# Optimization experiments

Hardware: AMD Instinct MI355X
Metric: run time of the kernel (lower is better)

The kernel has to match this reference:

```python
import jax, jax.numpy as jnp
import numpy as np

_MASK = -1.0e9
_EPS = 1e-8
B, N, E, D, L, NREL, TAU = 4, 2048, 32768, 128, 3, 1000, 0.1


def setup_inputs() -> dict:
    key = jax.random.key(0)
    ks = jax.random.split(key, 24)
    s = 0.05
    inp = {
        'edge_index': jax.random.randint(ks[0], (B, 2, E), 0, N, dtype=jnp.int32),
        'rels': jax.random.randint(ks[1], (B, E), 0, NREL, dtype=jnp.int32),
        'scores': jax.random.uniform(ks[2], (B, E), dtype=jnp.float32),
        'edge_conf_mask': jax.random.randint(ks[3], (B, E), 0, 2) > 0,
        'edge_mask': jax.random.randint(ks[4], (B, E), 0, 2) > 0,
        'mask': jnp.ones((B, N), dtype=bool),
        'r_query_embed': jax.random.normal(ks[5], (B, D), dtype=jnp.float32),
        'conf_embeds': jax.random.normal(ks[6], (B, E, D), dtype=jnp.float32),
        'rel_table': jax.random.normal(ks[7], (NREL, D), dtype=jnp.float32) * s,
        'beta_W': jax.random.normal(ks[8], (D, 1), dtype=jnp.float32) * s,
        'beta_b': jnp.zeros((1,), dtype=jnp.float32),
        'msg_W': jax.random.normal(ks[9], (L, 5 * D, D), dtype=jnp.float32) * s,
        'msg_b': jnp.zeros((L, D), dtype=jnp.float32),
        'upd_W': jax.random.normal(ks[10], (L, D, D), dtype=jnp.float32) * s,
        'upd_b': jnp.zeros((L, D), dtype=jnp.float32),
        'ln_g': jnp.ones((D,), dtype=jnp.float32),
        'ln_b': jnp.zeros((D,), dtype=jnp.float32),
        'att_W': jax.random.normal(ks[11], (L, 3 * D, 1), dtype=jnp.float32) * s,
        'att_b': jnp.zeros((L, 1), dtype=jnp.float32),
        'den_W1': jax.random.normal(ks[12], (3 * D, D), dtype=jnp.float32) * s,
        'den_b1': jnp.zeros((D,), dtype=jnp.float32),
        'den_W2': jax.random.normal(ks[13], (D, 1), dtype=jnp.float32) * s,
        'den_b2': jnp.zeros((1,), dtype=jnp.float32),
    }
    return inp


def _layer_norm(x, g, b, eps=1e-5):
    mu = jnp.mean(x, axis=-1, keepdims=True)
    var = jnp.var(x, axis=-1, keepdims=True)
    return (x - mu) * jax.lax.rsqrt(var + eps) * g + b


def reference(edge_index, rels, scores, edge_conf_mask, edge_mask, mask,
              r_query_embed, conf_embeds, rel_table, beta_W, beta_b,
              msg_W, msg_b, upd_W, upd_b, ln_g, ln_b, att_W, att_b,
              den_W1, den_b1, den_W2, den_b2):
    Bb, Nn = mask.shape
    Ee = edge_index.shape[2]
    d = rel_table.shape[1]
    bidx = jnp.arange(Bb)[:, None]                      # [B,1] batch index for scatter/gather
    src = edge_index[:, 0, :]                           # [B,E]
    tgt = edge_index[:, 1, :]                           # [B,E]

    h_init = jnp.zeros((Bb, Nn, d), dtype=rel_table.dtype).at[:, 0, :].set(1.0)
    h = h_init
    h_r = rel_table[rels]                               # [B,E,D]
    rq = jnp.broadcast_to(r_query_embed[:, None, :], (Bb, Ee, d))
    em = edge_mask.astype(h.dtype)[..., None]           # [B,E,1]

    # edge denoiser gate
    gate_in = jnp.concatenate([h_r, rq, conf_embeds], axis=-1)
    den = jax.nn.sigmoid(jax.nn.relu(gate_in @ den_W1 + den_b1) @ den_W2 + den_b2) * em

    beta = jax.nn.sigmoid((h_r + rq) @ beta_W + beta_b)             # [B,E,1]
    gate_known = jax.nn.sigmoid((scores[..., None] - beta) / TAU)
    gate = jnp.where(edge_conf_mask[..., None], gate_known, 0.5)

    outs = []
    for k in range(msg_W.shape[0]):
        h_src = h[bidx, src]                            # [B,E,D] gather
        h_init_src = h_init[bidx, src]
        msg_in = jnp.concatenate([h_src * h_r, h_src, h_init_src, h_r, conf_embeds], axis=-1)
        raw_msg = jax.nn.relu(msg_in @ msg_W[k] + msg_b[k])         # [B,E,D]

        att_in = jnp.concatenate([raw_msg, h_r, rq], axis=-1)
        att = jax.nn.leaky_relu((att_in @ att_W[k] + att_b[k])[..., 0], 0.01)
        att = jnp.where(edge_mask, att, _MASK)

        # scatter-softmax over edges sharing a target node
        mx = jnp.full((Bb, Nn), _MASK, dtype=att.dtype).at[bidx, tgt].max(att)
        ex = jnp.exp(att - mx[bidx, tgt])
        sm = jnp.zeros((Bb, Nn), dtype=att.dtype).at[bidx, tgt].add(ex)
        alpha = ex / (sm[bidx, tgt] + _EPS)             # [B,E]

        wmsg = gate * alpha[..., None] * raw_msg * em * den
        aggr = jnp.zeros_like(h).at[bidx, tgt].add(wmsg)
        h = _layer_norm(h + aggr @ upd_W[k] + upd_b[k], ln_g, ln_b)
        outs.append(h[:, 0, :])
    return jnp.stack(outs, axis=1)                      # [B,L,D]
```

## Files before the change

### kernel.cpp

```cpp
#include <hip/hip_runtime.h>
#include <stdint.h>
#include <math.h>

#define BB 4
#define NNODE 2048
#define NE 32768
#define DDIM 128
#define NL 3
#define NRELS 1000
#define MASKV -1000000000.0f

typedef unsigned short ushort_t;
typedef __attribute__((ext_vector_type(8))) short bfrag;
typedef __attribute__((ext_vector_type(4))) float f4;

__device__ __forceinline__ float sigf(float x){ return 1.0f/(1.0f+expf(-x)); }

__device__ __forceinline__ float bf2f(ushort_t u){
  union { unsigned int i; float f; } v; v.i = ((unsigned int)u) << 16; return v.f;
}
__device__ __forceinline__ ushort_t f2bf(float x){
  union { float f; unsigned int u; } v; v.f = x;
  unsigned int r = (v.u + 0x7FFFu + ((v.u >> 16) & 1u)) >> 16;
  return (ushort_t)r;
}
__device__ __forceinline__ float bflo(unsigned u){
  union{unsigned i;float f;}v; v.i=u<<16; return v.f;
}
__device__ __forceinline__ float bfhi(unsigned u){
  union{unsigned i;float f;}v; v.i=u&0xFFFF0000u; return v.f;
}
__device__ __forceinline__ unsigned pmul_bf(unsigned a, unsigned b){
  return (unsigned)f2bf(bflo(a)*bflo(b)) | ((unsigned)f2bf(bfhi(a)*bfhi(b))<<16);
}
__device__ __forceinline__ unsigned packbf(float a, float b){
  return (unsigned)f2bf(a) | ((unsigned)f2bf(b)<<16);
}

__global__ void prep_kernel(const void* cm_raw, const void* em_raw,
    uint8_t* __restrict__ cm, uint8_t* __restrict__ em, int* __restrict__ deg,
    const float* __restrict__ relt, ushort_t* __restrict__ relt_bf,
    const float* __restrict__ rq,
    const float* __restrict__ attW, const float* __restrict__ betaW,
    const float* __restrict__ msgW, const float* __restrict__ denW1,
    const float* __restrict__ denb1,
    int* __restrict__ src_c, int* __restrict__ rel_c, int* __restrict__ ge_c,
    float* __restrict__ h, ushort_t* __restrict__ h_bf,
    ushort_t* __restrict__ img_msg, ushort_t* __restrict__ img_den,
    ushort_t* __restrict__ img_tab,
    float* __restrict__ att_rel, float* __restrict__ att_rq,
    float* __restrict__ beta_rel, float* __restrict__ beta_rq,
    float* __restrict__ denrq, float* __restrict__ initvec,
    float* __restrict__ src0vec)
{
  __shared__ int flag_s;
  if (threadIdx.x < 64){
    unsigned v = ((const unsigned*)cm_raw)[threadIdx.x];
    bool i32ok = (v <= 1u);
    bool f32ok = (v == 0u) || (v == 0x3F800000u);
    unsigned long long bi = __ballot(i32ok);
    unsigned long long bf_ = __ballot(f32ok);
    if (threadIdx.x == 0) flag_s = (bi==~0ULL) ? 0 : ((bf_==~0ULL) ? 1 : 2);
  }
  __syncthreads();
  const int f = flag_s;
  const int gid = blockIdx.x*256 + threadIdx.x;

  if (gid < BB*NE){
    uint8_t c, e;
    if (f == 0){ c = ((const int*)cm_raw)[gid]!=0;   e = ((const int*)em_raw)[gid]!=0; }
    else if (f == 1){ c = ((const float*)cm_raw)[gid]!=0.0f; e = ((const float*)em_raw)[gid]!=0.0f; }
    else { c = ((const uint8_t*)cm_raw)[gid]!=0; e = ((const uint8_t*)em_raw)[gid]!=0; }
    cm[gid]=c; em[gid]=e;
    src_c[gid]=0; rel_c[gid]=0; ge_c[gid]=0;
  }
  if (gid < BB*NNODE) deg[gid]=0;
  if (gid < NRELS*DDIM/4){
    float4 v = *(const float4*)&relt[gid*4];
    ushort4 o; o.x=f2bf(v.x); o.y=f2bf(v.y); o.z=f2bf(v.z); o.w=f2bf(v.w);
    *(ushort4*)&relt_bf[gid*4] = o;
  }
  {
    int base = gid*4;
    int nd = base & (NNODE*DDIM - 1);
    bool one = (nd < DDIM);
    float4 hv = one ? (float4){1.f,1.f,1.f,1.f} : (float4){0.f,0.f,0.f,0.f};
    ushort4 hb = one ? (ushort4){0x3F80,0x3F80,0x3F80,0x3F80} : (ushort4){0,0,0,0};
    *(float4*)&h[base] = hv;
    *(ushort4*)&h_bf[base] = hb;
  }
  if (gid < 22*8192){
    int img_id = gid >> 13;
    int ei = gid & 8191;
    int j = ei >> 6;
    int kk = (((ei & 63) << 1) ^ ((j & 7) << 4)) >> 1;
    float v; ushort_t* dst;
    if (img_id < 12){
      int k = img_id >> 2, c = img_id & 3;
      int rowbase = (c < 2) ? c*64 : 512 + (c-2)*64;
      v = msgW[(size_t)k*81920 + (rowbase+kk)*128 + j];
      dst = img_msg + (size_t)img_id*8192;
    } else if (img_id < 14){
      int c = img_id - 12;
      v = denW1[(size_t)(256 + c*64 + kk)*128 + j];
      dst = img_den + (size_t)c*8192;
    } else if (img_id < 20){
      int idx = img_id - 14, k = idx >> 1, c = idx & 1;
      v = msgW[(size_t)k*81920 + (384 + c*64 + kk)*128 + j];
      dst = img_tab + (size_t)idx*8192;
    } else {
      int c = img_id - 20;
      v = denW1[(size_t)(c*64 + kk)*128 + j];
      dst = img_tab + (size_t)(6+c)*8192;
    }
    dst[ei] = f2bf(v);
  }
  {
    int wid = gid >> 6;
    int lane = threadIdx.x & 63;
    if (wid < 4016){
      const float* vec; const float* w; float* dst; int di;
      if (wid < 3*NRELS){
        int k = wid/1000, rl = wid%1000;
        vec = relt + rl*DDIM; w = attW + k*384 + 128; dst = att_rel; di = wid;
      } else if (wid < 3*NRELS + 3*BB){
        int idx = wid - 3*NRELS; int k = idx/BB, b = idx%BB;
        vec = rq + b*DDIM; w = attW + k*384 + 256; dst = att_rq; di = idx;
      } else if (wid < 3*NRELS + 3*BB + NRELS){
        int rl = wid - (3*NRELS + 3*BB);
        vec = relt + rl*DDIM; w = betaW; dst = beta_rel; di = rl;
      } else {
        int b = wid - (3*NRELS + 3*BB + NRELS);
        vec = rq + b*DDIM; w = betaW; dst = beta_rq; di = b;
      }
      float s = vec[lane]*w[lane] + vec[lane+64]*w[lane+64];
      #pragma unroll
      for (int off=32; off; off>>=1) s += __shfl_xor(s, off, 64);
      if (lane == 0) dst[di] = s;
    } else if (wid < 4024){
      int widx = wid - 4016;
      const float* A = nullptr; const float* W; int K = 128;
      float* outp; const float* bias = nullptr;
      if (widx < 4){ A = rq + widx*128; W = denW1 + 16384; outp = denrq + widx*128; bias = denb1; }
      else if (widx < 7){ int k=widx-4; W = msgW + (size_t)k*81920 + 32768; outp = initvec + k*128; }
      else { W = msgW + 16384; K = 256; outp = src0vec; }
      float a0=0.f, a1=0.f;
      for (int kk=0; kk<K; kk+=8){
        float av[8], w0[8], w1[8];
        #pragma unroll
        for (int u=0;u<8;++u){
          av[u] = A ? A[kk+u] : 1.0f;
          w0[u] = W[(size_t)(kk+u)*128 + lane];
          w1[u] = W[(size_t)(kk+u)*128 + lane + 64];
        }
        #pragma unroll
        for (int u=0;u<8;++u){ a0 = fmaf(av[u], w0[u], a0); a1 = fmaf(av[u], w1[u], a1); }
      }
      if (bias){ a0 += bias[lane]; a1 += bias[lane+64]; }
      outp[lane] = a0; outp[lane+64] = a1;
    }
  }
}

__global__ void csr_hist_kernel(const int* __restrict__ edge_index,
                                const uint8_t* __restrict__ em, int* __restrict__ deg){
  int gid = blockIdx.x*256 + threadIdx.x;
  if (!em[gid]) return;
  int b = gid >> 15, e = gid & (NE-1);
  int tgt = edge_index[(b<<16) + NE + e];
  atomicAdd(&deg[(b<<11) + tgt], 1);
}
__global__ void csr_scan_kernel(const int* __restrict__ deg,
                                int* __restrict__ base, int* __restrict__ cursor){
  __shared__ int part[256];
  int t = threadIdx.x;
  int loc[32]; int s = 0;
  #pragma unroll
  for (int i=0;i<32;++i){ loc[i] = deg[t*32+i]; s += loc[i]; }
  part[t] = s; __syncthreads();
  for (int off=1; off<256; off<<=1){
    int v = (t >= off) ? part[t-off] : 0;
    __syncthreads();
    part[t] += v;
    __syncthreads();
  }
  int ex = (t==0) ? 0 : part[t-1];
  #pragma unroll
  for (int i=0;i<32;++i){ base[t*32+i] = ex; cursor[t*32+i] = ex; ex += loc[i]; }
  if (t == 255) base[256*32] = ex;
}
__global__ void csr_scatter_kernel(const int* __restrict__ edge_index,
                                   const int* __restrict__ rels,
                                   const uint8_t* __restrict__ em,
                                   int* __restrict__ cursor,
                                   int* __restrict__ src_c, int* __restrict__ rel_c,
                                   int* __restrict__ ge_c){
  int gid = blockIdx.x*256 + threadIdx.x;
  if (!em[gid]) return;
  int b = gid >> 15, e = gid & (NE-1);
  int tgt = edge_index[(b<<16) + NE + e];
  int src = edge_index[(b<<16) + e];
  int pos = atomicAdd(&cursor[(b<<11) + tgt], 1);
  src_c[pos] = (b<<11) | src;
  rel_c[pos] = rels[gid];
  ge_c[pos]  = gid;
}

__global__ __launch_bounds__(256,2) void table_gemm_kernel(
    const ushort_t* __restrict__ relt_bf, const ushort_t* __restrict__ img_msg,
    const ushort_t* __restrict__ img_tab, const float* __restrict__ msgb,
    float* __restrict__ relmsg, float* __restrict__ relhh0,
    float* __restrict__ denrel)
{
  __shared__ char lds[32768];
  __shared__ float bias_s[128];
  const int blk = blockIdx.x;
  const int job = blk % 5;
  const int ri0 = (blk/5) << 7;
  const int t = threadIdx.x;
  const uint4* imgb;
  float* outp;
  if (job < 3){ imgb = (const uint4*)(img_tab + (size_t)(2*job)*8192); outp = relmsg + (size_t)job*NRELS*DDIM; }
  else if (job == 3){ imgb = (const uint4*)img_msg; outp = relhh0; }
  else { imgb = (const uint4*)(img_tab + (size_t)6*8192); outp = denrel; }
  if (t < 128) bias_s[t] = (job < 3) ? msgb[job*128 + t] : 0.f;

  const int lane=t&63, wid=t>>6;
  const int wr=wid>>1, wc=wid&1;
  const int rbase=wr<<6, cbase=wc<<6;
  const int lr=lane&15, lk=lane>>4;
  const int swz=(lane&7)<<4;
  const int g=t&7, row0=t>>3;
  const int aswz=(g<<4)^((row0&7)<<4);

  f4 acc[4][4];
  #pragma unroll
  for (int m=0;m<4;++m)
    #pragma unroll
    for (int n=0;n<4;++n) acc[m][n]=(f4){0.f,0.f,0.f,0.f};

  uint4 pa[4], pb[4];
  auto issueA = [&](int ch){
    #pragma unroll
    for (int i=0;i<4;++i){
      int rr = ri0 + row0 + (i<<5);
      rr = (rr < NRELS) ? rr : (NRELS-1);
      pa[i] = *(const uint4*)&relt_bf[(size_t)rr*128 + (ch<<6) + (g<<3)];
    }
    #pragma unroll
    for (int i=0;i<4;++i) pb[i] = imgb[ch*1024 + (i<<8) + t];
  };

  __syncthreads();
  issueA(0);
  #pragma unroll
  for (int ch=0; ch<2; ++ch){
    #pragma unroll
    for (int i=0;i<4;++i){
      int row = row0 + (i<<5);
      *(uint4*)(lds + row*128 + aswz) = pa[i];
    }
    *(uint4*)(lds+16384+(t<<4))        = pb[0];
    *(uint4*)(lds+16384+(t<<4)+4096)   = pb[1];
    *(uint4*)(lds+16384+(t<<4)+8192)   = pb[2];
    *(uint4*)(lds+16384+(t<<4)+12288)  = pb[3];
    __syncthreads();
    if (ch < 1) issueA(ch+1);
    #pragma unroll
    for (int s=0;s<2;++s){
      bfrag af[4], bfr[4];
      #pragma unroll
      for (int m=0;m<4;++m)
        af[m] = *(const bfrag*)(lds + (rbase+(m<<4)+lr)*128 + (((s<<6)+(lk<<4)) ^ swz));
      #pragma unroll
      for (int n=0;n<4;++n)
        bfr[n] = *(const bfrag*)(lds + 16384 + (cbase+(n<<4)+lr)*128 + (((s<<6)+(lk<<4)) ^ swz));
      #pragma unroll
      for (int m=0;m<4;++m)
        #pragma unroll
        for (int n=0;n<4;++n)
          acc[m][n] = __builtin_amdgcn_mfma_f32_16x16x32_bf16(af[m], bfr[n], acc[m][n], 0,0,0);
    }
    __syncthreads();
  }

  #pragma unroll
  for (int m=0;m<4;++m)
    #pragma unroll
    for (int n=0;n<4;++n){
      int col = cbase + (n<<4) + lr;
      float bv = bias_s[col];
      #pragma unroll
      for (int q=0;q<4;++q){
        int gr = ri0 + rbase + (m<<4) + (lk<<2) + q;
        if (gr < NRELS) outp[(size_t)gr*128 + col] = acc[m][n][q] + bv;
      }
    }
}

__global__ __launch_bounds__(256,2) void coef_mfma_kernel(
    const int* __restrict__ nact_p,
    const int* __restrict__ rel_c, const int* __restrict__ ge_c,
    const float* __restrict__ conf, const ushort_t* __restrict__ img_den,
    const float* __restrict__ denrel, const float* __restrict__ denrq,
    const float* __restrict__ denW2, const float* __restrict__ denb2,
    const float* __restrict__ scores, const uint8_t* __restrict__ cm,
    const float* __restrict__ beta_rel, const float* __restrict__ beta_rq,
    const float* __restrict__ betab,
    float* __restrict__ coef_c)
{
  __shared__ char lds[32768];
  __shared__ int rel_s[128], ge_s[128];
  __shared__ float w2_s[128];

  const int blk = blockIdx.x;
  const int ci0 = blk << 7;
  const int nact = *nact_p;
  if (ci0 >= nact) return;
  const int t = threadIdx.x;
  if (t < 128){ rel_s[t]=rel_c[ci0+t]; ge_s[t]=ge_c[ci0+t]; w2_s[t]=denW2[t]; }

  const int lane=t&63, wid=t>>6;
  const int wr=wid>>1, wc=wid&1;
  const int rbase=wr<<6, cbase=wc<<6;
  const int lr=lane&15, lk=lane>>4;
  const int swz=(lane&7)<<4;
  const int g=t&7, row0=t>>3;
  const int aswz=(g<<4)^((row0&7)<<4);

  f4 acc[4][4];
  #pragma unroll
  for (int m=0;m<4;++m)
    #pragma unroll
    for (int n=0;n<4;++n) acc[m][n]=(f4){0.f,0.f,0.f,0.f};

  const uint4* imgp = (const uint4*)img_den;
  float4 pf0[4], pf1[4];
  uint4 pb[4];
  __syncthreads();

  auto issueA = [&](int ch){
    const int d0=(ch&1)<<6;
    #pragma unroll
    for (int i=0;i<4;++i){
      int row=row0+(i<<5);
      const float* cp = conf + (((size_t)ge_s[row])<<7) + d0 + (g<<3);
      pf0[i]=*(const float4*)cp; pf1[i]=*(const float4*)(cp+4);
    }
    #pragma unroll
    for (int i=0;i<4;++i) pb[i]=imgp[ch*1024+(i<<8)+t];
  };

  issueA(0);
  #pragma unroll
  for (int ch=0; ch<2; ++ch){
    #pragma unroll
    for (int i=0;i<4;++i){
      int row=row0+(i<<5);
      uint4 val;
      val.x=packbf(pf0[i].x,pf0[i].y); val.y=packbf(pf0[i].z,pf0[i].w);
      val.z=packbf(pf1[i].x,pf1[i].y); val.w=packbf(pf1[i].z,pf1[i].w);
      *(uint4*)(lds + row*128 + aswz) = val;
    }
    *(uint4*)(lds+16384+(t<<4))        = pb[0];
    *(uint4*)(lds+16384+(t<<4)+4096)   = pb[1];
    *(uint4*)(lds+16384+(t<<4)+8192)   = pb[2];
    *(uint4*)(lds+16384+(t<<4)+12288)  = pb[3];
    __syncthreads();
    if (ch < 1) issueA(ch+1);
    #pragma unroll
    for (int s=0;s<2;++s){
      bfrag af[4], bfr[4];
      #pragma unroll
      for (int m=0;m<4;++m)
        af[m] = *(const bfrag*)(lds + (rbase+(m<<4)+lr)*128 + (((s<<6)+(lk<<4)) ^ swz));
      #pragma unroll
      for (int n=0;n<4;++n)
        bfr[n] = *(const bfrag*)(lds + 16384 + (cbase+(n<<4)+lr)*128 + (((s<<6)+(lk<<4)) ^ swz));
      #pragma unroll
      for (int m=0;m<4;++m)
        #pragma unroll
        for (int n=0;n<4;++n)
          acc[m][n] = __builtin_amdgcn_mfma_f32_16x16x32_bf16(af[m], bfr[n], acc[m][n], 0,0,0);
    }
    __syncthreads();
  }

  #pragma unroll
  for (int m=0;m<4;++m)
    #pragma unroll
    for (int n=0;n<4;++n)
      #pragma unroll
      for (int q=0;q<4;++q){
        int row=rbase+(m<<4)+(lk<<2)+q;
        int col=cbase+(n<<4)+lr;
        *(ushort_t*)(lds+(row<<8)+((col<<1)^((row&7)<<4))) = f2bf(acc[m][n][q]);
      }
  __syncthreads();

  #pragma unroll
  for (int i=0;i<8;++i){
    int u=t+(i<<8), row=u>>4, gg=u&15, c0=gg<<3;
    uint4 v = *(const uint4*)(lds+(row<<8)+((gg<<4)^((row&7)<<4)));
    float vv[8] = {bflo(v.x),bfhi(v.x),bflo(v.y),bfhi(v.y),
                   bflo(v.z),bfhi(v.z),bflo(v.w),bfhi(v.w)};
    int rel=rel_s[row], ge=ge_s[row], b=ge>>15;
    const float* dr = denrel + ((size_t)rel<<7) + c0;
    const float* dq = denrq + (b<<7) + c0;
    float part=0.f;
    #pragma unroll
    for (int j=0;j<8;++j){
      float m = fmaxf(vv[j] + dr[j] + dq[j], 0.f);
      part = fmaf(m, w2_s[c0+j], part);
    }
    #pragma unroll
    for (int off=1; off<16; off<<=1) part += __shfl_xor(part, off, 16);
    if (gg == 0){
      float den = sigf(part + denb2[0]);
      float beta = sigf(beta_rel[rel] + beta_rq[b] + betab[0]);
      float gt = cm[ge] ? sigf((scores[ge]-beta)*10.0f) : 0.5f;
      coef_c[ci0+row] = gt * den;
    }
  }
}

template<bool L0>
__global__ __launch_bounds__(256,2) void msg_mfma_kernel(
    const int* __restrict__ nact_p,
    const int* __restrict__ src_c, const int* __restrict__ rel_c,
    const int* __restrict__ ge_c,
    const ushort_t* __restrict__ relt_bf, const float* __restrict__ conf,
    const ushort_t* __restrict__ h_bf, const float* __restrict__ H1,
    const ushort_t* __restrict__ img_msg,
    const float* __restrict__ relmsg, const float* __restrict__ relhh0,
    const float* __restrict__ src0vec, const float* __restrict__ initvec,
    const float* __restrict__ attW, const float* __restrict__ attb,
    const float* __restrict__ att_rel, const float* __restrict__ att_rq,
    ushort_t* __restrict__ raw_c, float* __restrict__ att_c, int layer)
{
  constexpr int NCH = L0 ? 2 : 4;
  __shared__ char lds[32768];
  __shared__ int src_s[128], rel_s[128], ge_s[128];
  __shared__ float attw_s[128];

  const int blk = blockIdx.x;
  const int ci0 = blk << 7;
  const int nact = *nact_p;
  if (ci0 >= nact) return;
  const int t = threadIdx.x;
  if (t < 128){
    src_s[t]=src_c[ci0+t]; rel_s[t]=rel_c[ci0+t]; ge_s[t]=ge_c[ci0+t];
    attw_s[t]=attW[layer*384+t];
  }

  const int lane=t&63, wid=t>>6;
  const int wr=wid>>1, wc=wid&1;
  const int rbase=wr<<6, cbase=wc<<6;
  const int lr=lane&15, lk=lane>>4;
  const int swz=(lane&7)<<4;
  const int g=t&7, row0=t>>3;
  const int aswz=(g<<4)^((row0&7)<<4);

  f4 acc[4][4];
  #pragma unroll
  for (int m=0;m<4;++m)
    #pragma unroll
    for (int n=0;n<4;++n) acc[m][n]=(f4){0.f,0.f,0.f,0.f};

  const uint4* imgp = (const uint4*)(img_msg + (size_t)layer*4*8192);
  uint4 pa[4], pr[4], pb[4];
  float4 pf0[4], pf1[4];
  __syncthreads();

  auto issueA = [&](int ch){
    const int d0=(ch&1)<<6;
    const bool cf = L0 || (ch>=2);
    #pragma unroll
    for (int i=0;i<4;++i){
      int row=row0+(i<<5);
      if (cf){
        const float* cp = conf + (((size_t)ge_s[row])<<7) + d0 + (g<<3);
        pf0[i]=*(const float4*)cp; pf1[i]=*(const float4*)(cp+4);
      } else {
        pa[i]=*(const uint4*)&h_bf[(((size_t)src_s[row])<<7)+d0+(g<<3)];
        pr[i]=*(const uint4*)&relt_bf[(((size_t)rel_s[row])<<7)+d0+(g<<3)];
      }
    }
    int ic = L0 ? ch+2 : ch;
    #pragma unroll
    for (int i=0;i<4;++i) pb[i]=imgp[ic*1024+(i<<8)+t];
  };

  issueA(0);
  #pragma unroll
  for (int ch=0; ch<NCH; ++ch){
    const bool cf = L0 || (ch>=2);
    #pragma unroll
    for (int i=0;i<4;++i){
      int row=row0+(i<<5);
      uint4 val;
      if (cf){
        val.x=packbf(pf0[i].x,pf0[i].y); val.y=packbf(pf0[i].z,pf0[i].w);
        val.z=packbf(pf1[i].x,pf1[i].y); val.w=packbf(pf1[i].z,pf1[i].w);
      } else {
        val.x=pmul_bf(pa[i].x,pr[i].x); val.y=pmul_bf(pa[i].y,pr[i].y);
        val.z=pmul_bf(pa[i].z,pr[i].z); val.w=pmul_bf(pa[i].w,pr[i].w);
      }
      *(uint4*)(lds + row*128 + aswz) = val;
    }
    *(uint4*)(lds+16384+(t<<4))        = pb[0];
    *(uint4*)(lds+16384+(t<<4)+4096)   = pb[1];
    *(uint4*)(lds+16384+(t<<4)+8192)   = pb[2];
    *(uint4*)(lds+16384+(t<<4)+12288)  = pb[3];
    __syncthreads();
    if (ch < NCH-1) issueA(ch+1);
    #pragma unroll
    for (int s=0;s<2;++s){
      bfrag af[4], bfr[4];
      #pragma unroll
      for (int m=0;m<4;++m)
        af[m] = *(const bfrag*)(lds + (rbase+(m<<4)+lr)*128 + (((s<<6)+(lk<<4)) ^ swz));
      #pragma unroll
      for (int n=0;n<4;++n)
        bfr[n] = *(const bfrag*)(lds + 16384 + (cbase+(n<<4)+lr)*128 + (((s<<6)+(lk<<4)) ^ swz));
      #pragma unroll
      for (int m=0;m<4;++m)
        #pragma unroll
        for (int n=0;n<4;++n)
          acc[m][n] = __builtin_amdgcn_mfma_f32_16x16x32_bf16(af[m], bfr[n], acc[m][n], 0,0,0);
    }
    __syncthreads();
  }

  #pragma unroll
  for (int m=0;m<4;++m)
    #pragma unroll
    for (int n=0;n<4;++n)
      #pragma unroll
      for (int q=0;q<4;++q){
        int row=rbase+(m<<4)+(lk<<2)+q;
        int col=cbase+(n<<4)+lr;
        *(ushort_t*)(lds+(row<<8)+((col<<1)^((row&7)<<4))) = f2bf(acc[m][n][q]);
      }
  __syncthreads();

  #pragma unroll
  for (int i=0;i<8;++i){
    int u=t+(i<<8), row=u>>4, gg=u&15, c0=gg<<3;
    uint4 v = *(const uint4*)(lds+(row<<8)+((gg<<4)^((row&7)<<4)));
    float vv[8] = {bflo(v.x),bfhi(v.x),bflo(v.y),bfhi(v.y),
                   bflo(v.z),bfhi(v.z),bflo(v.w),bfhi(v.w)};
    int rel=rel_s[row], sc=src_s[row], ge=ge_s[row], b=ge>>15;
    const float* rm = relmsg + (((size_t)(layer*NRELS+rel))<<7) + c0;
    float bias[8];
    #pragma unroll
    for (int j=0;j<8;++j) bias[j] = rm[j];
    if (!L0){
      const float* hp = H1 + (((size_t)sc)<<7) + c0;
      #pragma unroll
      for (int j=0;j<8;++j) bias[j] += hp[j];
      if ((sc & (NNODE-1)) == 0){
        const float* iv = initvec + layer*128 + c0;
        #pragma unroll
        for (int j=0;j<8;++j) bias[j] += iv[j];
      }
    } else {
      if ((sc & (NNODE-1)) == 0){
        const float* rh = relhh0 + ((size_t)rel<<7) + c0;
        const float* sv = src0vec + c0;
        #pragma unroll
        for (int j=0;j<8;++j) bias[j] += rh[j] + sv[j];
      }
    }
    float part=0.f;
    unsigned o0,o1,o2,o3;
    {
      float m0=fmaxf(vv[0]+bias[0],0.f), m1=fmaxf(vv[1]+bias[1],0.f);
      float m2=fmaxf(vv[2]+bias[2],0.f), m3=fmaxf(vv[3]+bias[3],0.f);
      float m4=fmaxf(vv[4]+bias[4],0.f), m5=fmaxf(vv[5]+bias[5],0.f);
      float m6=fmaxf(vv[6]+bias[6],0.f), m7=fmaxf(vv[7]+bias[7],0.f);
      part = m0*attw_s[c0] + m1*attw_s[c0+1] + m2*attw_s[c0+2] + m3*attw_s[c0+3]
           + m4*attw_s[c0+4] + m5*attw_s[c0+5] + m6*attw_s[c0+6] + m7*attw_s[c0+7];
      o0=packbf(m0,m1); o1=packbf(m2,m3); o2=packbf(m4,m5); o3=packbf(m6,m7);
    }
    uint4 ov; ov.x=o0; ov.y=o1; ov.z=o2; ov.w=o3;
    *(uint4*)&raw_c[(((size_t)(ci0+row))<<7) + c0] = ov;
    #pragma unroll
    for (int off=1; off<16; off<<=1) part += __shfl_xor(part, off, 16);
    if (gg == 0){
      float a = part + att_rel[layer*NRELS+rel] + att_rq[layer*BB+b] + attb[layer];
      a = (a >= 0.f) ? a : 0.01f*a;
      att_c[ci0+row] = a;
    }
  }
}

__global__ __launch_bounds__(128) void node_agg_kernel(
    const int* __restrict__ base,
    const float* __restrict__ att_c, const float* __restrict__ coef_c,
    const ushort_t* __restrict__ raw_c, float* __restrict__ aggr)
{
  const int n = blockIdx.x;
  const int t = threadIdx.x;
  const int b0 = base[n], b1 = base[n+1];
  const int deg = b1 - b0;
  if (deg == 0){ aggr[((size_t)n<<7)+t] = 0.f; return; }
  __shared__ float w_s[128];
  __shared__ float red[4];
  float mx = -3.0e38f;
  for (int j=t; j<deg; j+=128) mx = fmaxf(mx, att_c[b0+j]);
  #pragma unroll
  for (int o=1;o<64;o<<=1) mx = fmaxf(mx, __shfl_xor(mx, o, 64));
  if ((t&63)==0) red[t>>6] = mx;
  __syncthreads();
  mx = fmaxf(red[0], red[1]);
  float s = 0.f;
  for (int j=t; j<deg; j+=128) s += expf(att_c[b0+j]-mx);
  #pragma unroll
  for (int o=1;o<64;o<<=1) s += __shfl_xor(s, o, 64);
  if ((t&63)==0) red[2+(t>>6)] = s;
  __syncthreads();
  const float inv = 1.0f/((red[2]+red[3]) + 1e-8f);
  float accv = 0.f;
  for (int jb=0; jb<deg; jb+=128){
    int jj = jb + t;
    __syncthreads();
    if (jj < deg) w_s[t] = coef_c[b0+jj] * expf(att_c[b0+jj]-mx) * inv;
    __syncthreads();
    int lim = min(128, deg-jb);
    int j = 0;
    for (; j+3 < lim; j += 4){
      float v0 = bf2f(raw_c[(((size_t)(b0+jb+j  ))<<7)+t]);
      float v1 = bf2f(raw_c[(((size_t)(b0+jb+j+1))<<7)+t]);
      float v2 = bf2f(raw_c[(((size_t)(b0+jb+j+2))<<7)+t]);
      float v3 = bf2f(raw_c[(((size_t)(b0+jb+j+3))<<7)+t]);
      accv = fmaf(w_s[j],v0,accv);
      accv = fmaf(w_s[j+1],v1,accv);
      accv = fmaf(w_s[j+2],v2,accv);
      accv = fmaf(w_s[j+3],v3,accv);
    }
    for (; j<lim; ++j)
      accv = fmaf(w_s[j], bf2f(raw_c[(((size_t)(b0+jb+j))<<7)+t]), accv);
  }
  aggr[((size_t)n<<7)+t] = accv;
}

#define FMA4(acc, a, bv) do { \
    acc.x = fmaf(a, bv.x, acc.x); \
    acc.y = fmaf(a, bv.y, acc.y); \
    acc.z = fmaf(a, bv.z, acc.z); \
    acc.w = fmaf(a, bv.w, acc.w); } while(0)

__global__ __launch_bounds__(256,2) void update_kernel(
    const float* __restrict__ aggr, const float* __restrict__ updW,
    const float* __restrict__ updb,
    const float* __restrict__ lng, const float* __restrict__ lnb,
    const float* __restrict__ msgW,
    float* __restrict__ h, ushort_t* __restrict__ h_bf,
    float* __restrict__ H1, float* __restrict__ out, int layer)
{
  __shared__ float As[64*65];
  __shared__ float Bs[64*128];
  const int t = threadIdx.x, blk = blockIdx.x;
  const int n0 = blk << 6;
  const int c = t & 15, r = t >> 4;
// ... 111 lines not shown
        Bs[(kk<<7)+j] = w1[((ch<<6)+kk)*DDIM + j];
      }
      __syncthreads();
      #pragma unroll 4
      for (int kk=0;kk<64;++kk){
        const float4 b0 = *(const float4*)&Bs[(kk<<7) + col0];
        const float4 b1 = *(const float4*)&Bs[(kk<<7) + 64 + col0];
        #pragma unroll
        for (int i=0;i<4;++i){
          const float a = As[((r<<2)+i)*65 + kk];
          FMA4(k0[i], a, b0);
          FMA4(k1[i], a, b1);
        }
      }
    }
    #pragma unroll
    for (int i=0;i<4;++i){
      const int row = n0 + (r<<2) + i;
      *(float4*)&H1[(size_t)row*DDIM + col0]      = k0[i];
      *(float4*)&H1[(size_t)row*DDIM + 64 + col0] = k1[i];
    }
  }
}

extern "C" void kernel_launch(void* const* d_in, const int* in_sizes, int n_in,
                              void* d_out, int out_size, void* d_ws, size_t ws_size,
                              hipStream_t stream) {
  const int*   edge_index = (const int*)d_in[0];
  const int*   rels       = (const int*)d_in[1];
  const float* scores     = (const float*)d_in[2];
  const void*  cm_raw     = d_in[3];
  const void*  em_raw     = d_in[4];
  const float* rq    = (const float*)d_in[6];
  const float* conf  = (const float*)d_in[7];
  const float* relt  = (const float*)d_in[8];
  const float* betaW = (const float*)d_in[9];
  const float* betab = (const float*)d_in[10];
  const float* msgW  = (const float*)d_in[11];
  const float* msgb  = (const float*)d_in[12];
  const float* updW  = (const float*)d_in[13];
  const float* updb  = (const float*)d_in[14];
  const float* lng   = (const float*)d_in[15];
  const float* lnb   = (const float*)d_in[16];
  const float* attW  = (const float*)d_in[17];
  const float* attb  = (const float*)d_in[18];
  const float* denW1 = (const float*)d_in[19];
  const float* denb1 = (const float*)d_in[20];
  const float* denW2 = (const float*)d_in[21];
  const float* denb2 = (const float*)d_in[22];
  float* out = (float*)d_out;
  char* ws = (char*)d_ws;

  size_t off = 0;
  float* h        = (float*)(ws + off); off += (size_t)BB*NNODE*DDIM*4;
  ushort_t* h_bf  = (ushort_t*)(ws + off); off += (size_t)BB*NNODE*DDIM*2;
  float* aggr     = (float*)(ws + off); off += (size_t)BB*NNODE*DDIM*4;
  float* H1       = (float*)(ws + off); off += (size_t)BB*NNODE*DDIM*4;
  ushort_t* raw_c = (ushort_t*)(ws + off); off += (size_t)BB*NE*DDIM*2;
  float* att_c    = (float*)(ws + off); off += (size_t)BB*NE*4;
  float* coef_c   = (float*)(ws + off); off += (size_t)BB*NE*4;
  int* src_c      = (int*)(ws + off); off += (size_t)BB*NE*4;
  int* rel_c      = (int*)(ws + off); off += (size_t)BB*NE*4;
  int* ge_c       = (int*)(ws + off); off += (size_t)BB*NE*4;
  int* deg        = (int*)(ws + off); off += (size_t)BB*NNODE*4;
  int* base       = (int*)(ws + off); off += (size_t)(BB*NNODE+16)*4;
  int* cursor     = (int*)(ws + off); off += (size_t)BB*NNODE*4;
  ushort_t* relt_bf = (ushort_t*)(ws + off); off += (size_t)NRELS*DDIM*2 + 64;
  ushort_t* img_msg = (ushort_t*)(ws + off); off += (size_t)12*8192*2;
  ushort_t* img_den = (ushort_t*)(ws + off); off += (size_t)2*8192*2;
  ushort_t* img_tab = (ushort_t*)(ws + off); off += (size_t)8*8192*2;
  float* relmsg   = (float*)(ws + off); off += (size_t)3*NRELS*DDIM*4;
  float* relhh0   = (float*)(ws + off); off += (size_t)NRELS*DDIM*4;
  float* denrel   = (float*)(ws + off); off += (size_t)NRELS*DDIM*4;
  float* denrq    = (float*)(ws + off); off += (size_t)BB*DDIM*4;
  float* initvec  = (float*)(ws + off); off += 3*DDIM*4;
  float* src0vec  = (float*)(ws + off); off += DDIM*4;
  float* att_rel  = (float*)(ws + off); off += 3*NRELS*4 + 32;
  float* att_rq   = (float*)(ws + off); off += 64;
  float* beta_rel = (float*)(ws + off); off += NRELS*4 + 32;
  float* beta_rq  = (float*)(ws + off); off += 64;
  uint8_t* cm_dec = (uint8_t*)(ws + off); off += (size_t)BB*NE;
  uint8_t* em_dec = (uint8_t*)(ws + off); off += (size_t)BB*NE;

  prep_kernel<<<1024, 256, 0, stream>>>(cm_raw, em_raw, cm_dec, em_dec, deg,
                                        relt, relt_bf, rq, attW, betaW,
                                        msgW, denW1, denb1,
                                        src_c, rel_c, ge_c, h, h_bf,
                                        img_msg, img_den, img_tab,
                                        att_rel, att_rq, beta_rel, beta_rq,
                                        denrq, initvec, src0vec);
  csr_hist_kernel<<<512, 256, 0, stream>>>(edge_index, em_dec, deg);
  csr_scan_kernel<<<1, 256, 0, stream>>>(deg, base, cursor);
  csr_scatter_kernel<<<512, 256, 0, stream>>>(edge_index, rels, em_dec, cursor,
                                              src_c, rel_c, ge_c);
  table_gemm_kernel<<<40, 256, 0, stream>>>(relt_bf, img_msg, img_tab, msgb,
                                            relmsg, relhh0, denrel);
  coef_mfma_kernel<<<1024, 256, 0, stream>>>(base + BB*NNODE, rel_c, ge_c, conf, img_den,
                                             denrel, denrq, denW2, denb2,
                                             scores, cm_dec, beta_rel, beta_rq, betab,
                                             coef_c);
  for (int k = 0; k < NL; ++k){
    if (k == 0){
      msg_mfma_kernel<true><<<1024, 256, 0, stream>>>(base + BB*NNODE, src_c, rel_c, ge_c,
          relt_bf, conf, h_bf, H1, img_msg, relmsg, relhh0, src0vec, initvec,
          attW, attb, att_rel, att_rq, raw_c, att_c, k);
    } else {
      msg_mfma_kernel<false><<<1024, 256, 0, stream>>>(base + BB*NNODE, src_c, rel_c, ge_c,
          relt_bf, conf, h_bf, H1, img_msg, relmsg, relhh0, src0vec, initvec,
          attW, attb, att_rel, att_rq, raw_c, att_c, k);
    }
    node_agg_kernel<<<BB*NNODE, 128, 0, stream>>>(base, att_c, coef_c, raw_c, aggr);
    update_kernel<<<128, 256, 0, stream>>>(aggr, updW, updb, lng, lnb, msgW,
                                           h, h_bf, H1, out, k);
  }
}
```

Measured before the change: 366.2 us.

## Merge CSR histogram, scatter, table GEMM and coef kernels to cut launches

```diff
diff --git a/kernel.cpp b/kernel.cpp
--- a/kernel.cpp
+++ b/kernel.cpp
@@ -38,6 +38,7 @@
 }
 
 __global__ void prep_kernel(const void* cm_raw, const void* em_raw,
+    const int* __restrict__ edge_index,
     uint8_t* __restrict__ cm, uint8_t* __restrict__ em, int* __restrict__ deg,
     const float* __restrict__ relt, ushort_t* __restrict__ relt_bf,
     const float* __restrict__ rq,
@@ -73,8 +74,12 @@
     else { c = ((const uint8_t*)cm_raw)[gid]!=0; e = ((const uint8_t*)em_raw)[gid]!=0; }
     cm[gid]=c; em[gid]=e;
     src_c[gid]=0; rel_c[gid]=0; ge_c[gid]=0;
-  }
-  if (gid < BB*NNODE) deg[gid]=0;
+    if (e){
+      int b = gid >> 15, ee = gid & (NE-1);
+      int tgt = edge_index[(b<<16) + NE + ee];
+      atomicAdd(&deg[(b<<11) + tgt], 1);
+    }
+  }
   if (gid < NRELS*DDIM/4){
     float4 v = *(const float4*)&relt[gid*4];
     ushort4 o; o.x=f2bf(v.x); o.y=f2bf(v.y); o.z=f2bf(v.z); o.w=f2bf(v.w);
@@ -162,14 +167,6 @@
   }
 }
 
-__global__ void csr_hist_kernel(const int* __restrict__ edge_index,
-                                const uint8_t* __restrict__ em, int* __restrict__ deg){
-  int gid = blockIdx.x*256 + threadIdx.x;
-  if (!em[gid]) return;
-  int b = gid >> 15, e = gid & (NE-1);
-  int tgt = edge_index[(b<<16) + NE + e];
-  atomicAdd(&deg[(b<<11) + tgt], 1);
-}
 __global__ void csr_scan_kernel(const int* __restrict__ deg,
                                 int* __restrict__ base, int* __restrict__ cursor){
   __shared__ int part[256];
@@ -189,41 +186,42 @@
   for (int i=0;i<32;++i){ base[t*32+i] = ex; cursor[t*32+i] = ex; ex += loc[i]; }
   if (t == 255) base[256*32] = ex;
 }
-__global__ void csr_scatter_kernel(const int* __restrict__ edge_index,
-                                   const int* __restrict__ rels,
-                                   const uint8_t* __restrict__ em,
-                                   int* __restrict__ cursor,
-                                   int* __restrict__ src_c, int* __restrict__ rel_c,
-                                   int* __restrict__ ge_c){
-  int gid = blockIdx.x*256 + threadIdx.x;
-  if (!em[gid]) return;
-  int b = gid >> 15, e = gid & (NE-1);
-  int tgt = edge_index[(b<<16) + NE + e];
-  int src = edge_index[(b<<16) + e];
-  int pos = atomicAdd(&cursor[(b<<11) + tgt], 1);
-  src_c[pos] = (b<<11) | src;
-  rel_c[pos] = rels[gid];
-  ge_c[pos]  = gid;
-}
-
-__global__ __launch_bounds__(256,2) void table_gemm_kernel(
+
+__global__ __launch_bounds__(256,2) void scatter_tab_kernel(
+    const int* __restrict__ edge_index, const int* __restrict__ rels,
+    const uint8_t* __restrict__ em, int* __restrict__ cursor,
+    int* __restrict__ src_c, int* __restrict__ rel_c, int* __restrict__ ge_c,
     const ushort_t* __restrict__ relt_bf, const ushort_t* __restrict__ img_msg,
     const ushort_t* __restrict__ img_tab, const float* __restrict__ msgb,
     float* __restrict__ relmsg, float* __restrict__ relhh0,
     float* __restrict__ denrel)
 {
   __shared__ char lds[32768];
-  __shared__ float bias_s[128];
-  const int blk = blockIdx.x;
+  __shared__ float fs0[128];
+  const int t = threadIdx.x;
+
+  if (blockIdx.x < 512){
+    int gid = blockIdx.x*256 + t;
+    if (!em[gid]) return;
+    int b = gid >> 15, e = gid & (NE-1);
+    int tgt = edge_index[(b<<16) + NE + e];
+    int src = edge_index[(b<<16) + e];
+    int pos = atomicAdd(&cursor[(b<<11) + tgt], 1);
+    src_c[pos] = (b<<11) | src;
+    rel_c[pos] = rels[gid];
+    ge_c[pos]  = gid;
+    return;
+  }
+
+  const int blk = blockIdx.x - 512;
   const int job = blk % 5;
   const int ri0 = (blk/5) << 7;
-  const int t = threadIdx.x;
   const uint4* imgb;
   float* outp;
   if (job < 3){ imgb = (const uint4*)(img_tab + (size_t)(2*job)*8192); outp = relmsg + (size_t)job*NRELS*DDIM; }
   else if (job == 3){ imgb = (const uint4*)img_msg; outp = relhh0; }
   else { imgb = (const uint4*)(img_tab + (size_t)6*8192); outp = denrel; }
-  if (t < 128) bias_s[t] = (job < 3) ? msgb[job*128 + t] : 0.f;
+  if (t < 128) fs0[t] = (job < 3) ? msgb[job*128 + t] : 0.f;
 
   const int lane=t&63, wid=t>>6;
   const int wr=wid>>1, wc=wid&1;
@@ -289,7 +287,7 @@
     #pragma unroll
     for (int n=0;n<4;++n){
       int col = cbase + (n<<4) + lr;
-      float bv = bias_s[col];
+      float bv = fs0[col];
       #pragma unroll
       for (int q=0;q<4;++q){
         int gr = ri0 + rbase + (m<<4) + (lk<<2) + q;
@@ -298,27 +296,36 @@
     }
 }
 
-__global__ __launch_bounds__(256,2) void coef_mfma_kernel(
+template<bool FUSED_L0>
+__global__ __launch_bounds__(256,2) void msg_mfma_kernel(
     const int* __restrict__ nact_p,
-    const int* __restrict__ rel_c, const int* __restrict__ ge_c,
-    const float* __restrict__ conf, const ushort_t* __restrict__ img_den,
+    const int* __restrict__ src_c, const int* __restrict__ rel_c,
+    const int* __restrict__ ge_c,
+    const ushort_t* __restrict__ relt_bf, const float* __restrict__ conf,
+    const ushort_t* __restrict__ h_bf, const float* __restrict__ H1,
+    const ushort_t* __restrict__ img_msg, const ushort_t* __restrict__ img_den,
+    const float* __restrict__ relmsg, const float* __restrict__ relhh0,
+    const float* __restrict__ src0vec, const float* __restrict__ initvec,
+    const float* __restrict__ attW, const float* __restrict__ attb,
+    const float* __restrict__ att_rel, const float* __restrict__ att_rq,
     const float* __restrict__ denrel, const float* __restrict__ denrq,
     const float* __restrict__ denW2, const float* __restrict__ denb2,
     const float* __restrict__ scores, const uint8_t* __restrict__ cm,
     const float* __restrict__ beta_rel, const float* __restrict__ beta_rq,
     const float* __restrict__ betab,
-    float* __restrict__ coef_c)
+    ushort_t* __restrict__ raw_c, float* __restrict__ att_c,
+    float* __restrict__ coef_c, int layer)
 {
   __shared__ char lds[32768];
-  __shared__ int rel_s[128], ge_s[128];
-  __shared__ float w2_s[128];
-
-  const int blk = blockIdx.x;
+  __shared__ int is0[128], is1[128], is2[128];
+  __shared__ float fs0[128];
+
+  const int t = threadIdx.x;
+  const int nact = *nact_p;
+  const bool is_coef = FUSED_L0 && (blockIdx.x >= 1024);
+  const int blk = is_coef ? (blockIdx.x - 1024) : blockIdx.x;
   const int ci0 = blk << 7;
-  const int nact = *nact_p;
   if (ci0 >= nact) return;
-  const int t = threadIdx.x;
-  if (t < 128){ rel_s[t]=rel_c[ci0+t]; ge_s[t]=ge_c[ci0+t]; w2_s[t]=denW2[t]; }
 
   const int lane=t&63, wid=t>>6;
   const int wr=wid>>1, wc=wid&1;
@@ -334,139 +341,105 @@
     #pragma unroll
     for (int n=0;n<4;++n) acc[m][n]=(f4){0.f,0.f,0.f,0.f};
 
-  const uint4* imgp = (const uint4*)img_den;
-  float4 pf0[4], pf1[4];
-  uint4 pb[4];
-  __syncthreads();
-
-  auto issueA = [&](int ch){
-    const int d0=(ch&1)<<6;
-    #pragma unroll
-    for (int i=0;i<4;++i){
-      int row=row0+(i<<5);
-      const float* cp = conf + (((size_t)ge_s[row])<<7) + d0 + (g<<3);
-      pf0[i]=*(const float4*)cp; pf1[i]=*(const float4*)(cp+4);
-    }
-    #pragma unroll
-    for (int i=0;i<4;++i) pb[i]=imgp[ch*1024+(i<<8)+t];
-  };
-
-  issueA(0);
-  #pragma unroll
-  for (int ch=0; ch<2; ++ch){
-    #pragma unroll
-    for (int i=0;i<4;++i){
-      int row=row0+(i<<5);
-      uint4 val;
-      val.x=packbf(pf0[i].x,pf0[i].y); val.y=packbf(pf0[i].z,pf0[i].w);
-      val.z=packbf(pf1[i].x,pf1[i].y); val.w=packbf(pf1[i].z,pf1[i].w);
-      *(uint4*)(lds + row*128 + aswz) = val;
-    }
-    *(uint4*)(lds+16384+(t<<4))        = pb[0];
-    *(uint4*)(lds+16384+(t<<4)+4096)   = pb[1];
-    *(uint4*)(lds+16384+(t<<4)+8192)   = pb[2];
-    *(uint4*)(lds+16384+(t<<4)+12288)  = pb[3];
-    __syncthreads();
-    if (ch < 1) issueA(ch+1);
-    #pragma unroll
-    for (int s=0;s<2;++s){
-      bfrag af[4], bfr[4];
-      #pragma unroll
-      for (int m=0;m<4;++m)
-        af[m] = *(const bfrag*)(lds + (rbase+(m<<4)+lr)*128 + (((s<<6)+(lk<<4)) ^ swz));
+  if (is_coef){
+    if (t < 128){ is1[t]=rel_c[ci0+t]; is2[t]=ge_c[ci0+t]; fs0[t]=denW2[t]; }
+    const uint4* imgp = (const uint4*)img_den;
+    float4 pf0[4], pf1[4];
+    uint4 pb[4];
+    __syncthreads();
+
+    auto issueA = [&](int ch){
+      const int d0=(ch&1)<<6;
+      #pragma unroll
+      for (int i=0;i<4;++i){
+        int row=row0+(i<<5);
+        const float* cp = conf + (((size_t)is2[row])<<7) + d0 + (g<<3);
+        pf0[i]=*(const float4*)cp; pf1[i]=*(const float4*)(cp+4);
+      }
+      #pragma unroll
+      for (int i=0;i<4;++i) pb[i]=imgp[ch*1024+(i<<8)+t];
+    };
+
+    issueA(0);
+    #pragma unroll
+    for (int ch=0; ch<2; ++ch){
+      #pragma unroll
+      for (int i=0;i<4;++i){
+        int row=row0+(i<<5);
+        uint4 val;
+        val.x=packbf(pf0[i].x,pf0[i].y); val.y=packbf(pf0[i].z,pf0[i].w);
+        val.z=packbf(pf1[i].x,pf1[i].y); val.w=packbf(pf1[i].z,pf1[i].w);
+        *(uint4*)(lds + row*128 + aswz) = val;
+      }
+      *(uint4*)(lds+16384+(t<<4))        = pb[0];
+      *(uint4*)(lds+16384+(t<<4)+4096)   = pb[1];
+      *(uint4*)(lds+16384+(t<<4)+8192)   = pb[2];
+      *(uint4*)(lds+16384+(t<<4)+12288)  = pb[3];
+      __syncthreads();
+      if (ch < 1) issueA(ch+1);
+      #pragma unroll
+      for (int s=0;s<2;++s){
+        bfrag af[4], bfr[4];
+        #pragma unroll
+        for (int m=0;m<4;++m)
+          af[m] = *(const bfrag*)(lds + (rbase+(m<<4)+lr)*128 + (((s<<6)+(lk<<4)) ^ swz));
+        #pragma unroll
+        for (int n=0;n<4;++n)
+          bfr[n] = *(const bfrag*)(lds + 16384 + (cbase+(n<<4)+lr)*128 + (((s<<6)+(lk<<4)) ^ swz));
+        #pragma unroll
+        for (int m=0;m<4;++m)
+          #pragma unroll
+          for (int n=0;n<4;++n)
+            acc[m][n] = __builtin_amdgcn_mfma_f32_16x16x32_bf16(af[m], bfr[n], acc[m][n], 0,0,0);
+      }
+      __syncthreads();
+    }
+
+    #pragma unroll
+    for (int m=0;m<4;++m)
       #pragma unroll
       for (int n=0;n<4;++n)
-        bfr[n] = *(const bfrag*)(lds + 16384 + (cbase+(n<<4)+lr)*128 + (((s<<6)+(lk<<4)) ^ swz));
-      #pragma unroll
-      for (int m=0;m<4;++m)
-        #pragma unroll
-        for (int n=0;n<4;++n)
-          acc[m][n] = __builtin_amdgcn_mfma_f32_16x16x32_bf16(af[m], bfr[n], acc[m][n], 0,0,0);
-    }
-    __syncthreads();
-  }
-
-  #pragma unroll
-  for (int m=0;m<4;++m)
-    #pragma unroll
-    for (int n=0;n<4;++n)
-      #pragma unroll
-      for (int q=0;q<4;++q){
-        int row=rbase+(m<<4)+(lk<<2)+q;
-        int col=cbase+(n<<4)+lr;
-        *(ushort_t*)(lds+(row<<8)+((col<<1)^((row&7)<<4))) = f2bf(acc[m][n][q]);
-      }
-  __syncthreads();
-
-  #pragma unroll
-  for (int i=0;i<8;++i){
-    int u=t+(i<<8), row=u>>4, gg=u&15, c0=gg<<3;
-    uint4 v = *(const uint4*)(lds+(row<<8)+((gg<<4)^((row&7)<<4)));
-    float vv[8] = {bflo(v.x),bfhi(v.x),bflo(v.y),bfhi(v.y),
-                   bflo(v.z),bfhi(v.z),bflo(v.w),bfhi(v.w)};
-    int rel=rel_s[row], ge=ge_s[row], b=ge>>15;
-    const float* dr = denrel + ((size_t)rel<<7) + c0;
-    const float* dq = denrq + (b<<7) + c0;
-    float part=0.f;
-    #pragma unroll
-    for (int j=0;j<8;++j){
-      float m = fmaxf(vv[j] + dr[j] + dq[j], 0.f);
-      part = fmaf(m, w2_s[c0+j], part);
-    }
-    #pragma unroll
-    for (int off=1; off<16; off<<=1) part += __shfl_xor(part, off, 16);
-    if (gg == 0){
-      float den = sigf(part + denb2[0]);
-      float beta = sigf(beta_rel[rel] + beta_rq[b] + betab[0]);
-      float gt = cm[ge] ? sigf((scores[ge]-beta)*10.0f) : 0.5f;
-      coef_c[ci0+row] = gt * den;
-    }
-  }
-}
-
-template<bool L0>
-__global__ __launch_bounds__(256,2) void msg_mfma_kernel(
-    const int* __restrict__ nact_p,
-    const int* __restrict__ src_c, const int* __restrict__ rel_c,
-    const int* __restrict__ ge_c,
-    const ushort_t* __restrict__ relt_bf, const float* __restrict__ conf,
-    const ushort_t* __restrict__ h_bf, const float* __restrict__ H1,
-    const ushort_t* __restrict__ img_msg,
-    const float* __restrict__ relmsg, const float* __restrict__ relhh0,
-    const float* __restrict__ src0vec, const float* __restrict__ initvec,
-    const float* __restrict__ attW, const float* __restrict__ attb,
-    const float* __restrict__ att_rel, const float* __restrict__ att_rq,
-    ushort_t* __restrict__ raw_c, float* __restrict__ att_c, int layer)
-{
-  constexpr int NCH = L0 ? 2 : 4;
-  __shared__ char lds[32768];
-  __shared__ int src_s[128], rel_s[128], ge_s[128];
-  __shared__ float attw_s[128];
-
-  const int blk = blockIdx.x;
-  const int ci0 = blk << 7;
-  const int nact = *nact_p;
-  if (ci0 >= nact) return;
-  const int t = threadIdx.x;
+        #pragma unroll
+        for (int q=0;q<4;++q){
+          int row=rbase+(m<<4)+(lk<<2)+q;
+          int col=cbase+(n<<4)+lr;
+          *(ushort_t*)(lds+(row<<8)+((col<<1)^((row&7)<<4))) = f2bf(acc[m][n][q]);
+        }
+    __syncthreads();
+
+    #pragma unroll
+    for (int i=0;i<8;++i){
+      int u=t+(i<<8), row=u>>4, gg=u&15, c0=gg<<3;
+      uint4 v = *(const uint4*)(lds+(row<<8)+((gg<<4)^((row&7)<<4)));
+      float vv[8] = {bflo(v.x),bfhi(v.x),bflo(v.y),bfhi(v.y),
+                     bflo(v.z),bfhi(v.z),bflo(v.w),bfhi(v.w)};
+      int rel=is1[row], ge=is2[row], b=ge>>15;
+      const float* dr = denrel + ((size_t)rel<<7) + c0;
+      const float* dq = denrq + (b<<7) + c0;
+      float part=0.f;
+      #pragma unroll
+      for (int j=0;j<8;++j){
+        float m = fmaxf(vv[j] + dr[j] + dq[j], 0.f);
+        part = fmaf(m, fs0[c0+j], part);
+      }
+      #pragma unroll
+      for (int off=1; off<16; off<<=1) part += __shfl_xor(part, off, 16);
+      if (gg == 0){
+        float den = sigf(part + denb2[0]);
+        float beta = sigf(beta_rel[rel] + beta_rq[b] + betab[0]);
+        float gt = cm[ge] ? sigf((scores[ge]-beta)*10.0f) : 0.5f;
+        coef_c[ci0+row] = gt * den;
+      }
+    }
+    return;
+  }
+
+  const bool L0 = FUSED_L0;
+  const int NCH = L0 ? 2 : 4;
   if (t < 128){
-    src_s[t]=src_c[ci0+t]; rel_s[t]=rel_c[ci0+t]; ge_s[t]=ge_c[ci0+t];
-    attw_s[t]=attW[layer*384+t];
-  }
-
-  const int lane=t&63, wid=t>>6;
-  const int wr=wid>>1, wc=wid&1;
-  const int rbase=wr<<6, cbase=wc<<6;
-  const int lr=lane&15, lk=lane>>4;
-  const int swz=(lane&7)<<4;
-  const int g=t&7, row0=t>>3;
-  const int aswz=(g<<4)^((row0&7)<<4);
-
-  f4 acc[4][4];
-  #pragma unroll
-  for (int m=0;m<4;++m)
-    #pragma unroll
-    for (int n=0;n<4;++n) acc[m][n]=(f4){0.f,0.f,0.f,0.f};
-
+    is0[t]=src_c[ci0+t]; is1[t]=rel_c[ci0+t]; is2[t]=ge_c[ci0+t];
+    fs0[t]=attW[layer*384+t];
+  }
   const uint4* imgp = (const uint4*)(img_msg + (size_t)layer*4*8192);
   uint4 pa[4], pr[4], pb[4];
   float4 pf0[4], pf1[4];
@@ -479,11 +452,11 @@
     for (int i=0;i<4;++i){
       int row=row0+(i<<5);
       if (cf){
-        const float* cp = conf + (((size_t)ge_s[row])<<7) + d0 + (g<<3);
+        const float* cp = conf + (((size_t)is2[row])<<7) + d0 + (g<<3);
         pf0[i]=*(const float4*)cp; pf1[i]=*(const float4*)(cp+4);
       } else {
-        pa[i]=*(const uint4*)&h_bf[(((size_t)src_s[row])<<7)+d0+(g<<3)];
-        pr[i]=*(const uint4*)&relt_bf[(((size_t)rel_s[row])<<7)+d0+(g<<3)];
+        pa[i]=*(const uint4*)&h_bf[(((size_t)is0[row])<<7)+d0+(g<<3)];
+        pr[i]=*(const uint4*)&relt_bf[(((size_t)is1[row])<<7)+d0+(g<<3)];
       }
     }
     int ic = L0 ? ch+2 : ch;
@@ -492,7 +465,6 @@
   };
 
   issueA(0);
-  #pragma unroll
   for (int ch=0; ch<NCH; ++ch){
     const bool cf = L0 || (ch>=2);
     #pragma unroll
@@ -550,7 +522,7 @@
     uint4 v = *(const uint4*)(lds+(row<<8)+((gg<<4)^((row&7)<<4)));
     float vv[8] = {bflo(v.x),bfhi(v.x),bflo(v.y),bfhi(v.y),
                    bflo(v.z),bfhi(v.z),bflo(v.w),bfhi(v.w)};
-    int rel=rel_s[row], sc=src_s[row], ge=ge_s[row], b=ge>>15;
+    int rel=is1[row], sc=is0[row], ge=is2[row], b=ge>>15;
     const float* rm = relmsg + (((size_t)(layer*NRELS+rel))<<7) + c0;
     float bias[8];
     #pragma unroll
@@ -579,8 +551,8 @@
       float m2=fmaxf(vv[2]+bias[2],0.f), m3=fmaxf(vv[3]+bias[3],0.f);
       float m4=fmaxf(vv[4]+bias[4],0.f), m5=fmaxf(vv[5]+bias[5],0.f);
       float m6=fmaxf(vv[6]+bias[6],0.f), m7=fmaxf(vv[7]+bias[7],0.f);
-      part = m0*attw_s[c0] + m1*attw_s[c0+1] + m2*attw_s[c0+2] + m3*attw_s[c0+3]
-           + m4*attw_s[c0+4] + m5*attw_s[c0+5] + m6*attw_s[c0+6] + m7*attw_s[c0+7];
+      part = m0*fs0[c0] + m1*fs0[c0+1] + m2*fs0[c0+2] + m3*fs0[c0+3]
+           + m4*fs0[c0+4] + m5*fs0[c0+5] + m6*fs0[c0+6] + m7*fs0[c0+7];
       o0=packbf(m0,m1); o1=packbf(m2,m3); o2=packbf(m4,m5); o3=packbf(m6,m7);
     }
     uint4 ov; ov.x=o0; ov.y=o1; ov.z=o2; ov.w=o3;
@@ -858,32 +830,33 @@
   uint8_t* cm_dec = (uint8_t*)(ws + off); off += (size_t)BB*NE;
   uint8_t* em_dec = (uint8_t*)(ws + off); off += (size_t)BB*NE;
 
-  prep_kernel<<<1024, 256, 0, stream>>>(cm_raw, em_raw, cm_dec, em_dec, deg,
+  hipMemsetAsync(deg, 0, (size_t)BB*NNODE*4, stream);
+  prep_kernel<<<1024, 256, 0, stream>>>(cm_raw, em_raw, edge_index,
+                                        cm_dec, em_dec, deg,
                                         relt, relt_bf, rq, attW, betaW,
                                         msgW, denW1, denb1,
                                         src_c, rel_c, ge_c, h, h_bf,
                                         img_msg, img_den, img_tab,
                                         att_rel, att_rq, beta_rel, beta_rq,
                                         denrq, initvec, src0vec);
-  csr_hist_kernel<<<512, 256, 0, stream>>>(edge_index, em_dec, deg);
   csr_scan_kernel<<<1, 256, 0, stream>>>(deg, base, cursor);
-  csr_scatter_kernel<<<512, 256, 0, stream>>>(edge_index, rels, em_dec, cursor,
-                                              src_c, rel_c, ge_c);
-  table_gemm_kernel<<<40, 256, 0, stream>>>(relt_bf, img_msg, img_tab, msgb,
-                                            relmsg, relhh0, denrel);
-  coef_mfma_kernel<<<1024, 256, 0, stream>>>(base + BB*NNODE, rel_c, ge_c, conf, img_den,
-                                             denrel, denrq, denW2, denb2,
-                                             scores, cm_dec, beta_rel, beta_rq, betab,
-                                             coef_c);
+  scatter_tab_kernel<<<552, 256, 0, stream>>>(edge_index, rels, em_dec, cursor,
+                                              src_c, rel_c, ge_c,
+                                              relt_bf, img_msg, img_tab, msgb,
+                                              relmsg, relhh0, denrel);
   for (int k = 0; k < NL; ++k){
     if (k == 0){
-      msg_mfma_kernel<true><<<1024, 256, 0, stream>>>(base + BB*NNODE, src_c, rel_c, ge_c,
-          relt_bf, conf, h_bf, H1, img_msg, relmsg, relhh0, src0vec, initvec,
-          attW, attb, att_rel, att_rq, raw_c, att_c, k);
+      msg_mfma_kernel<true><<<2048, 256, 0, stream>>>(base + BB*NNODE, src_c, rel_c, ge_c,
+          relt_bf, conf, h_bf, H1, img_msg, img_den, relmsg, relhh0, src0vec, initvec,
+          attW, attb, att_rel, att_rq,
+          denrel, denrq, denW2, denb2, scores, cm_dec, beta_rel, beta_rq, betab,
+          raw_c, att_c, coef_c, k);
     } else {
       msg_mfma_kernel<false><<<1024, 256, 0, stream>>>(base + BB*NNODE, src_c, rel_c, ge_c,
-          relt_bf, conf, h_bf, H1, img_msg, relmsg, relhh0, src0vec, initvec,
-          attW, attb, att_rel, att_rq, raw_c, att_c, k);
+          relt_bf, conf, h_bf, H1, img_msg, img_den, relmsg, relhh0, src0vec, initvec,
+          attW, attb, att_rel, att_rq,
+          denrel, denrq, denW2, denb2, scores, cm_dec, beta_rel, beta_rq, betab,
+          raw_c, att_c, coef_c, k);
     }
     node_agg_kernel<<<BB*NNODE, 128, 0, stream>>>(base, att_c, coef_c, raw_c, aggr);
     update_kernel<<<128, 256, 0, stream>>>(aggr, updW, updb, lng, lnb, msgW,
```

Result: no change. 361.6 us (-1.3%).
